# Kernel optimization log

Hardware: AMD Instinct MI355X
Metric: run time of the kernel (lower is better)

The kernel has to match this reference:

```python
import jax, jax.numpy as jnp
import numpy as np

B, L = 1024, 256
POOL, FM, HEAD, EMB = 4, 64, 64, 48  # input_size=256, pool_size=4 -> 64x64 maps


def _smooth(x, scale):
    # replicate-pad box filter of width 2*scale+1, via cumsum (single pass)
    w = 2 * scale + 1
    xp = jnp.pad(x, ((0, 0), (scale, scale)), mode='edge')          # (B, L+2s)
    c = jnp.pad(jnp.cumsum(xp, axis=1), ((0, 0), (1, 0)))           # (B, L+2s+1)
    return (c[:, w:] - c[:, :-w]) / w                               # (B, L)


def _picker(g, wmap, wbias, fcw, fcb):
    # g: (B, 256, 256) pairwise feature map
    b = g.shape[0]
    p = g.reshape(b, FM, POOL, FM, POOL).mean(axis=(2, 4))          # AvgPool2d(4): (B,64,64)
    h = jax.nn.elu(jnp.einsum('bij,hij->bh', p, wmap) + wbias)      # (B, head)
    return jax.nn.elu(h @ fcw.T + fcb)                              # (B, emb)


def setup_inputs() -> dict:
    key = jax.random.key(0)
    ks = jax.random.split(key, 16)
    x = jax.random.uniform(ks[0], (B, L), dtype=jnp.float32)
    d = {'x': x}
    for i, name in enumerate(['di', 'ndi', 'dd']):
        d[f'wm_{name}'] = jax.random.normal(ks[1 + 4 * i], (HEAD, FM, FM), jnp.float32)
        d[f'b_{name}'] = jax.random.normal(ks[2 + 4 * i], (HEAD,), jnp.float32)
        d[f'fcw_{name}'] = jax.random.normal(ks[3 + 4 * i], (EMB, HEAD), jnp.float32) * (1.0 / np.sqrt(HEAD))
        d[f'fcb_{name}'] = jax.random.normal(ks[4 + 4 * i], (EMB,), jnp.float32) * 0.01
    d['fc1_w'] = jax.random.normal(ks[13], (48, 3 * EMB), jnp.float32) * (1.0 / np.sqrt(3 * EMB))
    d['fc1_b'] = jax.random.normal(ks[14], (48,), jnp.float32) * 0.01
    d['fc2_w'] = jax.random.normal(ks[15], (20, 48), jnp.float32) * (1.0 / np.sqrt(48))
    d['fc2_b'] = jnp.zeros((20,), jnp.float32)
    return d


def reference(x, wm_di, b_di, fcw_di, fcb_di,
              wm_ndi, b_ndi, fcw_ndi, fcb_ndi,
              wm_dd, b_dd, fcw_dd, fcb_dd,
              fc1_w, fc1_b, fc2_w, fc2_b):
    sm = _smooth(x, 2)
    diff = jnp.diff(sm, axis=1, prepend=x[:, :1])                   # (B, L)
    xi, xj = x[:, :, None], x[:, None, :]
    DI = xj - xi                                                    # (B, L, L)
    NDI = DI / (xj + xi + 1e-5)
    DD = diff[:, None, :] - diff[:, :, None]
    e_di = _picker(DI, wm_di, b_di, fcw_di, fcb_di)
    e_ndi = _picker(NDI, wm_ndi, b_ndi, fcw_ndi, fcb_ndi)
    e_dd = _picker(DD, wm_dd, b_dd, fcw_dd, fcb_dd)
    emb = jnp.concatenate([e_di, e_ndi, e_dd], axis=1)              # (B, 144)
    emb = jax.nn.elu(emb @ fc1_w.T + fc1_b)
    return emb @ fc2_w.T + fc2_b                                    # (B, 20)
```

## Files before the change

kernel.cpp:

```cpp
#include <hip/hip_runtime.h>
#include <hip/hip_bf16.h>
#include <math.h>

typedef __attribute__((ext_vector_type(8))) short short8;
typedef __attribute__((ext_vector_type(4))) float floatx4;

#define WS_WREDT 0u
#define WS_WMAT  (1u << 20)

__device__ __forceinline__ float eluf(float v) {
  return v > 0.f ? v : __expf(v) - 1.f;
}

__device__ __forceinline__ unsigned short f2bf(float f) {
  __hip_bfloat16 h = __float2bfloat16(f);
  return *reinterpret_cast<unsigned short*>(&h);
}

__global__ __launch_bounds__(256) void prep_kernel(
    const float* __restrict__ wm_di,
    const float* __restrict__ wm_ndi,
    const float* __restrict__ wm_dd,
    char* __restrict__ ws) {
  __shared__ float sm[64 * 65];
  const int t = threadIdx.x;
  if (blockIdx.x < 128) {
    const int sel = blockIdx.x >> 6, h = blockIdx.x & 63;
    const float* w = (sel ? wm_dd : wm_di) + h * 4096;
#pragma unroll 4
    for (int i = 0; i < 16; ++i) {
      const int e = i * 256 + t;
      sm[(e >> 6) * 65 + (e & 63)] = w[e];
    }
    __syncthreads();
    if (t < 64) {
      float cs = 0.f, rs = 0.f;
#pragma unroll 8
      for (int I = 0; I < 64; ++I) {
        cs += sm[I * 65 + t];
        rs += sm[t * 65 + I];
      }
      ((float*)(ws + WS_WREDT))[sel * 4096 + t * 64 + h] = cs - rs;
    }
  } else {
    const int h = blockIdx.x - 128;
    const float* w = wm_ndi + h * 4096;
#pragma unroll 4
    for (int i = 0; i < 16; ++i) {
      const int e = i * 256 + t;
      sm[(e >> 6) * 65 + (e & 63)] = w[e];
    }
    __syncthreads();
    const int kstep = t >> 2, kc = t & 3;
    const int lane = kc * 16 + (h & 15);
    const int n = h >> 4;
    short8 sv;
#pragma unroll
    for (int j = 0; j < 8; ++j) {
      const int k = kstep * 32 + kc * 8 + j;
      const int I = k >> 5, tt = k & 31;
      const int J = (I + 1 + tt) & 63;
      float v = 0.f;
      if (!(tt == 31 && I >= 32))
        v = 0.0625f * (sm[I * 65 + J] - sm[J * 65 + I]);
      sv[j] = (short)f2bf(v);
    }
    *(short8*)((__hip_bfloat16*)(ws + WS_WMAT) + (((n * 64 + kstep) * 64 + lane) << 3)) = sv;
  }
}

__global__ __launch_bounds__(1024, 8) void fused_kernel(
    const float* __restrict__ x,
    const float* __restrict__ b_di, const float* __restrict__ b_ndi,
    const float* __restrict__ b_dd,
    const float* __restrict__ fcw_di, const float* __restrict__ fcb_di,
    const float* __restrict__ fcw_ndi, const float* __restrict__ fcb_ndi,
    const float* __restrict__ fcw_dd, const float* __restrict__ fcb_dd,
    const float* __restrict__ fc1_w, const float* __restrict__ fc1_b,
    const float* __restrict__ fc2_w, const float* __restrict__ fc2_b,
    const char* __restrict__ ws,
    float* __restrict__ out) {
  __shared__ float xs[2][256];
  __shared__ __align__(16) unsigned short ldsA[2][2][2048];
  __shared__ float pxs[2][64], pds[2][64];
  __shared__ float hp[16][4][2][16];
  __shared__ float hh[3][2][64];
  __shared__ float emb_s[2][144];
  __shared__ float f1v_s[2][48];

  const int t = threadIdx.x;
  const int b0 = blockIdx.x * 2;
  const float* __restrict__ wredT = (const float*)(ws + WS_WREDT);
  const short* __restrict__ wmaT = (const short*)(ws + WS_WMAT);

  if (t < 512) xs[t >> 8][t & 255] = x[(b0 + (t >> 8)) * 256 + (t & 255)];
  __syncthreads();

  if (t < 128) {
    const int r = t >> 6, m = t & 63;
    const float* __restrict__ xr = xs[r];
    const int b4 = 4 * m;
    pxs[r][m] = 0.25f * (xr[b4] + xr[b4 + 1] + xr[b4 + 2] + xr[b4 + 3]);
    const int i3 = min(b4 + 4, 255), i4 = min(b4 + 5, 255);
    const float smv = 0.2f * (xr[b4 + 1] + xr[b4 + 2] + xr[b4 + 3] + xr[i3] + xr[i4]);
    float prev = __shfl_up(smv, 1, 64);
    if (m == 0) prev = xr[0];
    pds[r][m] = 0.25f * (smv - prev);
  }

  {
    const int r = t >> 9;
    const int e0 = (t & 511) * 4;
    const int I = e0 >> 5;
    const float4 xiv = *(const float4*)&xs[r][I << 2];
    float ua[4], Ga[4];
    {
      const float ya[4] = {xiv.x, xiv.y, xiv.z, xiv.w};
#pragma unroll
      for (int a = 0; a < 4; ++a) {
        ua[a] = ya[a] + 1e-5f;
        Ga[a] = 2.f * ya[a] * ua[a];
      }
    }
#pragma unroll
    for (int i = 0; i < 4; ++i) {
      const int e = e0 + i;
      const int J = (I + 1 + (e & 31)) & 63;
      const float4 xjv = *(const float4*)&xs[r][J << 2];
      const float P01 = 2.f * xjv.x * xjv.y + (xjv.x + xjv.y) * 1e-5f;
      const float P23 = 2.f * xjv.z * xjv.w + (xjv.z + xjv.w) * 1e-5f;
      float s = 0.f;
#pragma unroll
      for (int a = 0; a < 4; ++a) {
        const float D0 = (xjv.x + ua[a]) * (xjv.y + ua[a]);
        const float D1 = (xjv.z + ua[a]) * (xjv.w + ua[a]);
        s += (P01 - Ga[a]) * __builtin_amdgcn_rcpf(D0);
        s += (P23 - Ga[a]) * __builtin_amdgcn_rcpf(D1);
      }
      const unsigned short hi = f2bf(s);
      union { unsigned int uu; float f; } hv; hv.uu = ((unsigned int)hi) << 16;
      ldsA[0][r][e] = hi;
      ldsA[1][r][e] = f2bf(s - hv.f);
    }
  }
  __syncthreads();

  {
    const int kh = t >> 6, lane = t & 63;
    const int arow = lane & 1;
    const int kofs = kh * 128 + ((lane >> 4) << 3);
    floatx4 acc0 = {0.f, 0.f, 0.f, 0.f}, acc1 = {0.f, 0.f, 0.f, 0.f};
    floatx4 acc2 = {0.f, 0.f, 0.f, 0.f}, acc3 = {0.f, 0.f, 0.f, 0.f};
#pragma unroll
    for (int s = 0; s < 4; ++s) {
      const int kk = kofs + s * 32;
      const short8 ah = *(const short8*)&ldsA[0][arow][kk];
      const short8 al = *(const short8*)&ldsA[1][arow][kk];
      const int base = ((kh * 4 + s) * 64 + lane) << 3;
      const short8 bv0 = *(const short8*)(wmaT + base);
      const short8 bv1 = *(const short8*)(wmaT + base + 32768);
      const short8 bv2 = *(const short8*)(wmaT + base + 65536);
      const short8 bv3 = *(const short8*)(wmaT + base + 98304);
      acc0 = __builtin_amdgcn_mfma_f32_16x16x32_bf16(ah, bv0, acc0, 0, 0, 0);
      acc0 = __builtin_amdgcn_mfma_f32_16x16x32_bf16(al, bv0, acc0, 0, 0, 0);
      acc1 = __builtin_amdgcn_mfma_f32_16x16x32_bf16(ah, bv1, acc1, 0, 0, 0);
      acc1 = __builtin_amdgcn_mfma_f32_16x16x32_bf16(al, bv1, acc1, 0, 0, 0);
      acc2 = __builtin_amdgcn_mfma_f32_16x16x32_bf16(ah, bv2, acc2, 0, 0, 0);
      acc2 = __builtin_amdgcn_mfma_f32_16x16x32_bf16(al, bv2, acc2, 0, 0, 0);
      acc3 = __builtin_amdgcn_mfma_f32_16x16x32_bf16(ah, bv3, acc3, 0, 0, 0);
      acc3 = __builtin_amdgcn_mfma_f32_16x16x32_bf16(al, bv3, acc3, 0, 0, 0);
    }
    if (lane < 16) {
      hp[kh][0][0][lane] = acc0[0]; hp[kh][0][1][lane] = acc0[1];
      hp[kh][1][0][lane] = acc1[0]; hp[kh][1][1][lane] = acc1[1];
      hp[kh][2][0][lane] = acc2[0]; hp[kh][2][1][lane] = acc2[1];
      hp[kh][3][0][lane] = acc3[0]; hp[kh][3][1][lane] = acc3[1];
    }
  }

  if (t < 128) {
    const int r = t >> 6, h = t & 63;
    float adi = b_di[h], add_ = b_dd[h];
#pragma unroll 8
    for (int K = 0; K < 64; ++K) {
      adi += pxs[r][K] * wredT[K * 64 + h];
      add_ += pds[r][K] * wredT[4096 + K * 64 + h];
    }
    hh[0][r][h] = eluf(adi);
    hh[2][r][h] = eluf(add_);
  }
  __syncthreads();

  if (t < 128) {
    const int row = t >> 6, h = t & 63;
    const int n = h >> 4, c = h & 15;
    float v = b_ndi[h];
#pragma unroll
    for (int kh = 0; kh < 16; ++kh) v += hp[kh][n][row][c];
    hh[1][row][h] = eluf(v);
  }
  __syncthreads();

  if (t < 2 * 144) {
    const int r = t / 144;
    const int k = t - r * 144;
    const int pick = k / 48;
    const int e = k - pick * 48;
    const float* __restrict__ fw = (pick == 0) ? fcw_di : (pick == 1) ? fcw_ndi : fcw_dd;
    const float* __restrict__ fb = (pick == 0) ? fcb_di : (pick == 1) ? fcb_ndi : fcb_dd;
    float a = fb[e];
#pragma unroll 8
    for (int hq = 0; hq < 64; ++hq) a += hh[pick][r][hq] * fw[e * 64 + hq];
    emb_s[r][k] = eluf(a);
  }
  __syncthreads();

  if (t < 2 * 48) {
    const int r = t / 48, o = t - (t / 48) * 48;
    float a = fc1_b[o];
#pragma unroll 8
    for (int k = 0; k < 144; ++k) a += emb_s[r][k] * fc1_w[o * 144 + k];
    f1v_s[r][o] = eluf(a);
  }
  __syncthreads();

  if (t < 2 * 20) {
    const int r = t / 20, o = t - (t / 20) * 20;
    float a = fc2_b[o];
#pragma unroll
    for (int j = 0; j < 48; ++j) a += f1v_s[r][j] * fc2_w[o * 48 + j];
    out[(b0 + r) * 20 + o] = a;
  }
}

extern "C" void kernel_launch(void* const* d_in, const int* in_sizes, int n_in,
                              void* d_out, int out_size, void* d_ws, size_t ws_size,
                              hipStream_t stream) {
  const float* x       = (const float*)d_in[0];
  const float* wm_di   = (const float*)d_in[1];
  const float* b_di    = (const float*)d_in[2];
  const float* fcw_di  = (const float*)d_in[3];
  const float* fcb_di  = (const float*)d_in[4];
  const float* wm_ndi  = (const float*)d_in[5];
  const float* b_ndi   = (const float*)d_in[6];
  const float* fcw_ndi = (const float*)d_in[7];
  const float* fcb_ndi = (const float*)d_in[8];
  const float* wm_dd   = (const float*)d_in[9];
  const float* b_dd    = (const float*)d_in[10];
  const float* fcw_dd  = (const float*)d_in[11];
  const float* fcb_dd  = (const float*)d_in[12];
  const float* fc1_w   = (const float*)d_in[13];
  const float* fc1_b   = (const float*)d_in[14];
  const float* fc2_w   = (const float*)d_in[15];
  const float* fc2_b   = (const float*)d_in[16];
  float* out = (float*)d_out;
  char* ws = (char*)d_ws;

  prep_kernel<<<192, 256, 0, stream>>>(wm_di, wm_ndi, wm_dd, ws);
  fused_kernel<<<512, 1024, 0, stream>>>(
      x, b_di, b_ndi, b_dd,
      fcw_di, fcb_di, fcw_ndi, fcb_ndi, fcw_dd, fcb_dd,
      fc1_w, fc1_b, fc2_w, fc2_b, ws, out);
}
```

Before: 27.97 us.

## Process four batch rows per block and stage small weights in LDS

Each block now handles four batch rows instead of two. Every MFMA call fills four A rows instead of two, so each B-fragment load from the bf16 weight matrix serves twice as much work, and the grid halves to 256 blocks. The prep kernel also writes transposed fc weights, fc1 weights and all biases into the workspace, and the fused kernel copies them together with the reduced wmap into about 99KB of shared memory for coalesced reuse. The cost is a large per-block LDS footprint that limits occupancy, extra copy traffic per block, and only 256 blocks to spread across the GPU.

```diff
diff --git a/kernel.cpp b/kernel.cpp
--- a/kernel.cpp
+++ b/kernel.cpp
@@ -5,7 +5,10 @@
 typedef __attribute__((ext_vector_type(8))) short short8;
 typedef __attribute__((ext_vector_type(4))) float floatx4;
 
-#define WS_WREDT 0u
+#define TP_FCW   8192
+#define TP_FC1   17408
+#define TP_BIAS  24320
+#define TP_N     24704
 #define WS_WMAT  (1u << 20)
 
 __device__ __forceinline__ float eluf(float v) {
@@ -21,11 +24,20 @@
     const float* __restrict__ wm_di,
     const float* __restrict__ wm_ndi,
     const float* __restrict__ wm_dd,
+    const float* __restrict__ b_di, const float* __restrict__ b_ndi,
+    const float* __restrict__ b_dd,
+    const float* __restrict__ fcw_di, const float* __restrict__ fcw_ndi,
+    const float* __restrict__ fcw_dd,
+    const float* __restrict__ fcb_di, const float* __restrict__ fcb_ndi,
+    const float* __restrict__ fcb_dd,
+    const float* __restrict__ fc1_w, const float* __restrict__ fc1_b,
     char* __restrict__ ws) {
   __shared__ float sm[64 * 65];
   const int t = threadIdx.x;
-  if (blockIdx.x < 128) {
-    const int sel = blockIdx.x >> 6, h = blockIdx.x & 63;
+  float* wsf = (float*)ws;
+  const int b = blockIdx.x;
+  if (b < 128) {
+    const int sel = b >> 6, h = b & 63;
     const float* w = (sel ? wm_dd : wm_di) + h * 4096;
 #pragma unroll 4
     for (int i = 0; i < 16; ++i) {
@@ -40,10 +52,10 @@
         cs += sm[I * 65 + t];
         rs += sm[t * 65 + I];
       }
-      ((float*)(ws + WS_WREDT))[sel * 4096 + t * 64 + h] = cs - rs;
-    }
-  } else {
-    const int h = blockIdx.x - 128;
+      wsf[sel * 4096 + t * 64 + h] = cs - rs;
+    }
+  } else if (b < 192) {
+    const int h = b - 128;
     const float* w = wm_ndi + h * 4096;
 #pragma unroll 4
     for (int i = 0; i < 16; ++i) {
@@ -66,37 +78,63 @@
       sv[j] = (short)f2bf(v);
     }
     *(short8*)((__hip_bfloat16*)(ws + WS_WMAT) + (((n * 64 + kstep) * 64 + lane) << 3)) = sv;
-  }
-}
-
-__global__ __launch_bounds__(1024, 8) void fused_kernel(
+  } else if (b < 195) {
+    const int pick = b - 192;
+    const float* src = (pick == 0) ? fcw_di : (pick == 1) ? fcw_ndi : fcw_dd;
+    for (int i = t; i < 3072; i += 256) {
+      const int e = i >> 6, hq = i & 63;
+      wsf[TP_FCW + pick * 3072 + hq * 48 + e] = src[i];
+    }
+  } else if (b == 195) {
+    for (int i = t; i < 6912; i += 256) {
+      const int o = i / 144, k = i - o * 144;
+      wsf[TP_FC1 + k * 48 + o] = fc1_w[i];
+    }
+  } else {
+    for (int i = t; i < 384; i += 256) {
+      float v;
+      if (i < 64) v = b_di[i];
+      else if (i < 128) v = b_ndi[i - 64];
+      else if (i < 192) v = b_dd[i - 128];
+      else if (i < 240) v = fcb_di[i - 192];
+      else if (i < 288) v = fcb_ndi[i - 240];
+      else if (i < 336) v = fcb_dd[i - 288];
+      else v = fc1_b[i - 336];
+      wsf[TP_BIAS + i] = v;
+    }
+  }
+}
+
+__global__ __launch_bounds__(1024, 4) void fused_kernel(
     const float* __restrict__ x,
-    const float* __restrict__ b_di, const float* __restrict__ b_ndi,
-    const float* __restrict__ b_dd,
-    const float* __restrict__ fcw_di, const float* __restrict__ fcb_di,
-    const float* __restrict__ fcw_ndi, const float* __restrict__ fcb_ndi,
-    const float* __restrict__ fcw_dd, const float* __restrict__ fcb_dd,
-    const float* __restrict__ fc1_w, const float* __restrict__ fc1_b,
     const float* __restrict__ fc2_w, const float* __restrict__ fc2_b,
     const char* __restrict__ ws,
     float* __restrict__ out) {
-  __shared__ float xs[2][256];
-  __shared__ __align__(16) unsigned short ldsA[2][2][2048];
-  __shared__ float pxs[2][64], pds[2][64];
-  __shared__ float hp[16][4][2][16];
-  __shared__ float hh[3][2][64];
-  __shared__ float emb_s[2][144];
-  __shared__ float f1v_s[2][48];
+  __shared__ float xs[4][256];
+  __shared__ __align__(16) unsigned short ldsA[2][4][2048];
+  __shared__ float pxs[4][64], pds[4][64];
+  __shared__ float hp[16][4][4][16];
+  __shared__ float hh[3][4][64];
+  __shared__ float emb_s[4][144];
+  __shared__ float f1v_s[4][48];
+  __shared__ __align__(16) float tp[TP_N];
 
   const int t = threadIdx.x;
-  const int b0 = blockIdx.x * 2;
-  const float* __restrict__ wredT = (const float*)(ws + WS_WREDT);
+  const int b0 = blockIdx.x * 4;
   const short* __restrict__ wmaT = (const short*)(ws + WS_WMAT);
-
-  if (t < 512) xs[t >> 8][t & 255] = x[(b0 + (t >> 8)) * 256 + (t & 255)];
-  __syncthreads();
-
-  if (t < 128) {
+  const float4* __restrict__ ws4 = (const float4*)ws;
+  float4* __restrict__ tp4 = (float4*)tp;
+
+  xs[t >> 8][t & 255] = x[(b0 + (t >> 8)) * 256 + (t & 255)];
+  __syncthreads();
+
+#pragma unroll
+  for (int j = 0; j < 7; ++j) {
+    const int idx = t + j * 1024;
+    if (idx < TP_N / 4) tp4[idx] = ws4[idx];
+  }
+
+  if (t < 256) {
     const int r = t >> 6, m = t & 63;
     const float* __restrict__ xr = xs[r];
     const int b4 = 4 * m;
@@ -108,9 +146,11 @@
     pds[r][m] = 0.25f * (smv - prev);
   }
 
-  {
-    const int r = t >> 9;
-    const int e0 = (t & 511) * 4;
+#pragma unroll
+  for (int gi = 0; gi < 2; ++gi) {
+    const int g = t + gi * 1024;
+    const int r = g >> 9;
+    const int e0 = (g & 511) * 4;
     const int I = e0 >> 5;
     const float4 xiv = *(const float4*)&xs[r][I << 2];
     float ua[4], Ga[4];
@@ -147,7 +187,7 @@
 
   {
     const int kh = t >> 6, lane = t & 63;
-    const int arow = lane & 1;
+    const int arow = (lane & 15) & 3;
     const int kofs = kh * 128 + ((lane >> 4) << 3);
     floatx4 acc0 = {0.f, 0.f, 0.f, 0.f}, acc1 = {0.f, 0.f, 0.f, 0.f};
     floatx4 acc2 = {0.f, 0.f, 0.f, 0.f}, acc3 = {0.f, 0.f, 0.f, 0.f};
@@ -171,60 +211,62 @@
       acc3 = __builtin_amdgcn_mfma_f32_16x16x32_bf16(al, bv3, acc3, 0, 0, 0);
     }
     if (lane < 16) {
-      hp[kh][0][0][lane] = acc0[0]; hp[kh][0][1][lane] = acc0[1];
-      hp[kh][1][0][lane] = acc1[0]; hp[kh][1][1][lane] = acc1[1];
-      hp[kh][2][0][lane] = acc2[0]; hp[kh][2][1][lane] = acc2[1];
-      hp[kh][3][0][lane] = acc3[0]; hp[kh][3][1][lane] = acc3[1];
-    }
-  }
-
-  if (t < 128) {
+#pragma unroll
+      for (int r = 0; r < 4; ++r) {
+        hp[kh][0][r][lane] = acc0[r];
+        hp[kh][1][r][lane] = acc1[r];
+        hp[kh][2][r][lane] = acc2[r];
+        hp[kh][3][r][lane] = acc3[r];
+      }
+    }
+  }
+
+  if (t < 256) {
     const int r = t >> 6, h = t & 63;
-    float adi = b_di[h], add_ = b_dd[h];
+    float adi = tp[TP_BIAS + h], add_ = tp[TP_BIAS + 128 + h];
 #pragma unroll 8
     for (int K = 0; K < 64; ++K) {
-      adi += pxs[r][K] * wredT[K * 64 + h];
-      add_ += pds[r][K] * wredT[4096 + K * 64 + h];
+      adi += pxs[r][K] * tp[K * 64 + h];
+      add_ += pds[r][K] * tp[4096 + K * 64 + h];
     }
     hh[0][r][h] = eluf(adi);
     hh[2][r][h] = eluf(add_);
   }
   __syncthreads();
 
-  if (t < 128) {
+  if (t < 256) {
     const int row = t >> 6, h = t & 63;
     const int n = h >> 4, c = h & 15;
-    float v = b_ndi[h];
+    float v = tp[TP_BIAS + 64 + h];
 #pragma unroll
     for (int kh = 0; kh < 16; ++kh) v += hp[kh][n][row][c];
     hh[1][row][h] = eluf(v);
   }
   __syncthreads();
 
-  if (t < 2 * 144) {
+  if (t < 4 * 144) {
     const int r = t / 144;
     const int k = t - r * 144;
     const int pick = k / 48;
     const int e = k - pick * 48;
-    const float* __restrict__ fw = (pick == 0) ? fcw_di : (pick == 1) ? fcw_ndi : fcw_dd;
-    const float* __restrict__ fb = (pick == 0) ? fcb_di : (pick == 1) ? fcb_ndi : fcb_dd;
-    float a = fb[e];
+    const float* __restrict__ fwt = tp + TP_FCW + pick * 3072;
+    float a = tp[TP_BIAS + 192 + pick * 48 + e];
 #pragma unroll 8
-    for (int hq = 0; hq < 64; ++hq) a += hh[pick][r][hq] * fw[e * 64 + hq];
+    for (int hq = 0; hq < 64; ++hq) a += hh[pick][r][hq] * fwt[hq * 48 + e];
     emb_s[r][k] = eluf(a);
   }
   __syncthreads();
 
-  if (t < 2 * 48) {
+  if (t < 4 * 48) {
     const int r = t / 48, o = t - (t / 48) * 48;
-    float a = fc1_b[o];
+    float a = tp[TP_BIAS + 336 + o];
 #pragma unroll 8
-    for (int k = 0; k < 144; ++k) a += emb_s[r][k] * fc1_w[o * 144 + k];
+    for (int k = 0; k < 144; ++k) a += emb_s[r][k] * tp[TP_FC1 + k * 48 + o];
     f1v_s[r][o] = eluf(a);
   }
   __syncthreads();
 
-  if (t < 2 * 20) {
+  if (t < 4 * 20) {
     const int r = t / 20, o = t - (t / 20) * 20;
     float a = fc2_b[o];
 #pragma unroll
@@ -256,9 +298,9 @@
   float* out = (float*)d_out;
   char* ws = (char*)d_ws;
 
-  prep_kernel<<<192, 256, 0, stream>>>(wm_di, wm_ndi, wm_dd, ws);
-  fused_kernel<<<512, 1024, 0, stream>>>(
-      x, b_di, b_ndi, b_dd,
-      fcw_di, fcb_di, fcw_ndi, fcb_ndi, fcw_dd, fcb_dd,
-      fc1_w, fc1_b, fc2_w, fc2_b, ws, out);
-}
+  prep_kernel<<<197, 256, 0, stream>>>(
+      wm_di, wm_ndi, wm_dd, b_di, b_ndi, b_dd,
+      fcw_di, fcw_ndi, fcw_dd, fcb_di, fcb_ndi, fcb_dd,
+      fc1_w, fc1_b, ws);
+  fused_kernel<<<256, 1024, 0, stream>>>(x, fc2_w, fc2_b, ws, out);
+}
```

New measurement: 26.23 us. -6.2%, faster.
